# Kernel tuning notes

Hardware: AMD Instinct MI355X
Metric: run time of the kernel (lower is better)

Reference implementation:

```python
import jax, jax.numpy as jnp
import numpy as np
import math

B, S, H = 8, 1024, 1024
NH, DH = 16, 64  # MULTI_HEAD, HIDDEN_SIZE_HEAD


def setup_inputs() -> dict:
    key = jax.random.key(0)
    ks = jax.random.split(key, 12)
    scale = 0.02
    inp = {
        "v": jax.random.normal(ks[0], (B, S, H), jnp.float32),
        "k": jax.random.normal(ks[1], (B, S, H), jnp.float32),
        "q": jax.random.normal(ks[2], (B, S, H), jnp.float32),
        # True = masked position (masked_fill semantics)
        "mask": jax.random.bernoulli(ks[3], 0.1, (B, 1, 1, S)),
        "Wq": jax.random.normal(ks[4], (H, H), jnp.float32) * scale,
        "bq": jnp.zeros((H,), jnp.float32),
        "Wk": jax.random.normal(ks[5], (H, H), jnp.float32) * scale,
        "bk": jnp.zeros((H,), jnp.float32),
        "Wv": jax.random.normal(ks[6], (H, H), jnp.float32) * scale,
        "bv": jnp.zeros((H,), jnp.float32),
        "Wm": jax.random.normal(ks[7], (H, H), jnp.float32) * scale,
        "bm": jnp.zeros((H,), jnp.float32),
    }
    return inp


def _split_heads(x):
    # [B, S, H] -> [B, NH, S, DH]
    b, s, _ = x.shape
    return x.reshape(b, s, NH, DH).transpose(0, 2, 1, 3)


def reference(v, k, q, mask, Wq, bq, Wk, bk, Wv, bv, Wm, bm):
    # QKV projections (torch Linear: x @ W.T + b)
    qh = _split_heads(q @ Wq.T + bq)  # [B, NH, S, DH]
    kh = _split_heads(k @ Wk.T + bk)
    vh = _split_heads(v @ Wv.T + bv)

    scores = jnp.einsum("bhqd,bhkd->bhqk", qh, kh) / math.sqrt(DH)
    scores = jnp.where(mask, jnp.float32(-1e9), scores)
    att = jax.nn.softmax(scores, axis=-1)
    # dropout rate 0.0 (eval mode) -> identity
    ctx = jnp.einsum("bhqk,bhkd->bhqd", att, vh)  # [B, NH, S, DH]

    b = q.shape[0]
    merged = ctx.transpose(0, 2, 1, 3).reshape(b, -1, NH * DH)  # [B, S, H]
    return merged @ Wm.T + bm
```

## Files before the change

kernel.cpp:

```cpp
#include <hip/hip_runtime.h>
#include <hip/hip_bf16.h>

#define Bn 8
#define Sn 1024
#define Hn 1024
#define NHn 16
#define DHn 64
#define Mn (Bn * Sn)

typedef unsigned short u16;
typedef short bf16x8 __attribute__((ext_vector_type(8)));
typedef unsigned short u16x4 __attribute__((ext_vector_type(4)));
typedef float f32x4 __attribute__((ext_vector_type(4)));

__device__ __forceinline__ u16 f2bf(float x) {
  union { __hip_bfloat16 h; u16 u; } cv;
  cv.h = __float2bfloat16(x);
  return cv.u;
}

__device__ __forceinline__ void async_ld16(void* lds, const void* g) {
  __builtin_amdgcn_global_load_lds(
      (const __attribute__((address_space(1))) void*)g,
      (__attribute__((address_space(3))) void*)lds, 16, 0, 0);
}

__global__ __launch_bounds__(256) void sniff_k(const void* __restrict__ mask,
                                               int* __restrict__ flags) {
  __shared__ int viol;
  if (threadIdx.x == 0) viol = 0;
  __syncthreads();
  const unsigned* mw = (const unsigned*)mask;
  int vb = 0;
#pragma unroll
  for (int j = 0; j < 8; ++j) {
    unsigned v = mw[threadIdx.x * 8 + j];
    if (v > 1u) vb |= 1;
    if ((v & 0xFEFEFEFEu) != 0u) vb |= 2;
    if (!(v == 0u || v == 0x3F800000u)) vb |= 4;
    unsigned h0 = v & 0xFFFFu, h1 = v >> 16;
    if (!((h0 == 0u || h0 == 0x3F80u) && (h1 == 0u || h1 == 0x3F80u))) vb |= 8;
  }
  if (vb) atomicOr(&viol, vb);
  __syncthreads();
  if (threadIdx.x == 0) {
    int mt;
    if (!(viol & 1))      mt = 0;
    else if (!(viol & 2)) mt = 1;
    else if (!(viol & 4)) mt = 3;
    else if (!(viol & 8)) mt = 2;
    else                  mt = 0;
    flags[1] = mt;
  }
}

__global__ __launch_bounds__(256) void convert3(
    const float* __restrict__ a, const float* __restrict__ b,
    const float* __restrict__ c, u16* __restrict__ da,
    u16* __restrict__ db, u16* __restrict__ dc) {
  const int seg = blockIdx.x >> 12;
  const int bid = blockIdx.x & 4095;
  const float* s = seg == 0 ? a : seg == 1 ? b : c;
  u16* d        = seg == 0 ? da : seg == 1 ? db : dc;
  const int i = (bid * 256 + threadIdx.x) * 8;
  f32x4 lo = *(const f32x4*)(s + i);
  f32x4 hi = *(const f32x4*)(s + i + 4);
  bf16x8 o;
#pragma unroll
  for (int j = 0; j < 4; ++j) { o[j] = (short)f2bf(lo[j]); o[4 + j] = (short)f2bf(hi[j]); }
  *(bf16x8*)(d + i) = o;
}

__global__ __launch_bounds__(256) void convertW(
    const float* __restrict__ a, const float* __restrict__ b,
    const float* __restrict__ c, const float* __restrict__ e,
    u16* __restrict__ da, u16* __restrict__ db,
    u16* __restrict__ dc, u16* __restrict__ de) {
  const int seg = blockIdx.x >> 9;
  const int bid = blockIdx.x & 511;
  const float* s = seg == 0 ? a : seg == 1 ? b : seg == 2 ? c : e;
  u16* d        = seg == 0 ? da : seg == 1 ? db : seg == 2 ? dc : de;
  const int i = (bid * 256 + threadIdx.x) * 8;
  f32x4 lo = *(const f32x4*)(s + i);
  f32x4 hi = *(const f32x4*)(s + i + 4);
  bf16x8 o;
#pragma unroll
  for (int j = 0; j < 4; ++j) { o[j] = (short)f2bf(lo[j]); o[4 + j] = (short)f2bf(hi[j]); }
  *(bf16x8*)(d + i) = o;
}

template <int OMODE>
__global__ __launch_bounds__(256) void gemm_bt(
    const u16* __restrict__ X, const u16* __restrict__ W,
    const float* __restrict__ bias, void* __restrict__ O, float scale)
{
  __shared__ __attribute__((aligned(16))) u16 As[128 * 32];
  __shared__ __attribute__((aligned(16))) u16 Bs[128 * 32];
  const int tid  = threadIdx.x;
  const int wave = tid >> 6;
  const int lane = tid & 63;
  const int ln   = lane & 15;
  const int quad = lane >> 4;
  const int m0 = blockIdx.x * 128;
  const int n0 = blockIdx.y * 128;
  const int wm = (wave & 1) * 64;
  const int wn = (wave >> 1) * 64;
  const int r0 = tid >> 2;
  const int oc = (tid & 3) * 8;
  char* A0 = (char*)As + wave * 1024;
  char* A1 = (char*)As + 4096 + wave * 1024;
  char* B0 = (char*)Bs + wave * 1024;
  char* B1 = (char*)Bs + 4096 + wave * 1024;

  f32x4 acc[4][4] = {};

  for (int k0 = 0; k0 < 1024; k0 += 32) {
    async_ld16(A0, X + (size_t)(m0 + r0) * 1024 + k0 + oc);
    async_ld16(A1, X + (size_t)(m0 + 64 + r0) * 1024 + k0 + oc);
    async_ld16(B0, W + (size_t)(n0 + r0) * 1024 + k0 + oc);
    async_ld16(B1, W + (size_t)(n0 + 64 + r0) * 1024 + k0 + oc);
    __syncthreads();
    bf16x8 af[4], bf[4];
#pragma unroll
    for (int t = 0; t < 4; ++t)
      af[t] = *(const bf16x8*)&As[(wm + t * 16 + ln) * 32 + quad * 8];
#pragma unroll
    for (int t = 0; t < 4; ++t)
      bf[t] = *(const bf16x8*)&Bs[(wn + t * 16 + ln) * 32 + quad * 8];
#pragma unroll
    for (int i = 0; i < 4; ++i)
#pragma unroll
      for (int j = 0; j < 4; ++j)
        acc[i][j] = __builtin_amdgcn_mfma_f32_16x16x32_bf16(af[i], bf[j], acc[i][j], 0, 0, 0);
    __syncthreads();
  }

  if (OMODE == 2) {
    const int bb = m0 >> 10;
    const int sb = m0 & 1023;
#pragma unroll
    for (int j = 0; j < 4; ++j) {
      const int col = n0 + wn + j * 16 + ln;
      const float bv = bias[col];
#pragma unroll
      for (int i = 0; i < 4; ++i) {
        const int sl = sb + wm + i * 16 + quad * 4;
        u16x4 pk;
#pragma unroll
        for (int r = 0; r < 4; ++r) pk[r] = f2bf((acc[i][j][r] + bv) * scale);
        *(u16x4*)&((u16*)O)[((size_t)(bb * 1024 + col)) * 1024 + sl] = pk;
      }
    }
  } else {
#pragma unroll
    for (int j = 0; j < 4; ++j) {
      const int col = n0 + wn + j * 16 + ln;
      const float bv = bias[col];
#pragma unroll
      for (int i = 0; i < 4; ++i) {
        const int rowb = m0 + wm + i * 16 + quad * 4;
#pragma unroll
        for (int r = 0; r < 4; ++r) {
          const float val = (acc[i][j][r] + bv) * scale;
          const size_t idx = (size_t)(rowb + r) * 1024 + col;
          if (OMODE == 1) ((float*)O)[idx] = val;
          else            ((u16*)O)[idx]   = f2bf(val);
        }
      }
    }
  }
}

__global__ __launch_bounds__(256) void attn(
    const u16* __restrict__ Qb, const u16* __restrict__ Kb,
    const u16* __restrict__ Vbt, const void* __restrict__ mask,
    const int* __restrict__ flags, u16* __restrict__ Ctx)
{
  __shared__ __attribute__((aligned(16))) u16 Ks[128 * 72];
  __shared__ __attribute__((aligned(16))) u16 Vt[64 * 136];
  __shared__ __attribute__((aligned(16))) u16 Pl[4][16 * 136];
  __shared__ __attribute__((aligned(16))) float maskf[Sn];

  const int tid  = threadIdx.x;
  const int wave = tid >> 6;
  const int lane = tid & 63;
  const int ln   = lane & 15;
  const int quad = lane >> 4;
  const int qt = blockIdx.x & 15;
  const int bh = blockIdx.x >> 4;
  const int b  = bh >> 4;
  const int h  = bh & 15;

  const int mt = flags[1];
  for (int i = tid; i < Sn; i += 256) {
    const int idx = b * Sn + i;
    int nz;
    if (mt == 0)      nz = ((const int*)mask)[idx] != 0;
    else if (mt == 1) nz = ((const signed char*)mask)[idx] != 0;
    else if (mt == 2) nz = ((const u16*)mask)[idx] != 0;
    else              nz = ((const unsigned*)mask)[idx] != 0;
    maskf[i] = nz ? -1e9f : 0.0f;
  }

  const size_t qoff = (size_t)(b * Sn + qt * 64 + wave * 16 + ln) * Hn + h * DHn;
  bf16x8 qf0 = *(const bf16x8*)&Qb[qoff + quad * 8];
  bf16x8 qf1 = *(const bf16x8*)&Qb[qoff + 32 + quad * 8];

  float mrun[4], lrun[4];
#pragma unroll
  for (int r = 0; r < 4; ++r) { mrun[r] = -INFINITY; lrun[r] = 0.0f; }
  f32x4 acc[4] = {};

  const int kr = tid >> 1, kh = tid & 1;
  const int vd = tid >> 2, vs = tid & 3;
  u16* pw = Pl[wave];

  for (int t8 = 0; t8 < 8; ++t8) {
    const int kv0 = t8 * 128;
    __syncthreads();
    {
      const u16* g = &Kb[(size_t)(b * Sn + kv0 + kr) * Hn + h * DHn + kh * 32];
      u16* l = &Ks[kr * 72 + kh * 32];
#pragma unroll
      for (int j = 0; j < 4; ++j) *(bf16x8*)(l + j * 8) = *(const bf16x8*)(g + j * 8);
    }
    {
      const u16* g = &Vbt[(size_t)(b * Sn + h * DHn + vd) * Sn + kv0 + vs * 32];
      u16* l = &Vt[vd * 136 + vs * 32];
#pragma unroll
      for (int j = 0; j < 4; ++j) *(bf16x8*)(l + j * 8) = *(const bf16x8*)(g + j * 8);
    }
    __syncthreads();

    f32x4 sc[8];
#pragma unroll
    for (int t = 0; t < 8; ++t) {
      const int row = (t * 16 + ln) * 72;
      bf16x8 kf0 = *(const bf16x8*)&Ks[row + quad * 8];
      bf16x8 kf1 = *(const bf16x8*)&Ks[row + 32 + quad * 8];
      f32x4 z = {};
      z = __builtin_amdgcn_mfma_f32_16x16x32_bf16(qf0, kf0, z, 0, 0, 0);
      z = __builtin_amdgcn_mfma_f32_16x16x32_bf16(qf1, kf1, z, 0, 0, 0);
      sc[t] = z;
    }
    float mf[8];
#pragma unroll
    for (int t = 0; t < 8; ++t) mf[t] = maskf[kv0 + t * 16 + ln];
#pragma unroll
    for (int t = 0; t < 8; ++t)
#pragma unroll
      for (int r = 0; r < 4; ++r) sc[t][r] += mf[t];

    float al[4], mx[4];
#pragma unroll
    for (int r = 0; r < 4; ++r) {
      float v = sc[0][r];
#pragma unroll
      for (int t = 1; t < 8; ++t) v = fmaxf(v, sc[t][r]);
      v = fmaxf(v, __shfl_xor(v, 1));
      v = fmaxf(v, __shfl_xor(v, 2));
      v = fmaxf(v, __shfl_xor(v, 4));
      v = fmaxf(v, __shfl_xor(v, 8));
      const float mnew = fmaxf(mrun[r], v);
      al[r] = __expf(mrun[r] - mnew);
      mrun[r] = mnew;
      mx[r] = mnew;
    }
#pragma unroll
    for (int r = 0; r < 4; ++r) {
      float s = 0.0f;
#pragma unroll
      for (int t = 0; t < 8; ++t) {
        const float p = __expf(sc[t][r] - mx[r]);
        sc[t][r] = p;
        s += p;
      }
      s += __shfl_xor(s, 1);
      s += __shfl_xor(s, 2);
      s += __shfl_xor(s, 4);
      s += __shfl_xor(s, 8);
      lrun[r] = lrun[r] * al[r] + s;
    }
#pragma unroll
    for (int t = 0; t < 8; ++t)
#pragma unroll
      for (int r = 0; r < 4; ++r)
        pw[(quad * 4 + r) * 136 + t * 16 + ln] = f2bf(sc[t][r]);
    __syncthreads();
#pragma unroll
    for (int dt = 0; dt < 4; ++dt)
#pragma unroll
      for (int r = 0; r < 4; ++r) acc[dt][r] *= al[r];
    bf16x8 pa[4];
#pragma unroll
    for (int c = 0; c < 4; ++c)
      pa[c] = *(const bf16x8*)&pw[ln * 136 + c * 32 + quad * 8];
#pragma unroll
    for (int dt = 0; dt < 4; ++dt) {
      const int vrow = (dt * 16 + ln) * 136;
#pragma unroll
      for (int c = 0; c < 4; ++c) {
        bf16x8 vb = *(const bf16x8*)&Vt[vrow + c * 32 + quad * 8];
        acc[dt] = __builtin_amdgcn_mfma_f32_16x16x32_bf16(pa[c], vb, acc[dt], 0, 0, 0);
      }
    }
  }

#pragma unroll
  for (int dt = 0; dt < 4; ++dt)
#pragma unroll
    for (int r = 0; r < 4; ++r) {
      const int s = qt * 64 + wave * 16 + quad * 4 + r;
      Ctx[(size_t)(b * Sn + s) * Hn + h * DHn + dt * 16 + ln] = f2bf(acc[dt][r] / lrun[r]);
    }
}

extern "C" void kernel_launch(void* const* d_in, const int* in_sizes, int n_in,
                              void* d_out, int out_size, void* d_ws, size_t ws_size,
                              hipStream_t stream) {
  const float* v    = (const float*)d_in[0];
  const float* k    = (const float*)d_in[1];
  const float* q    = (const float*)d_in[2];
  const void*  mask = d_in[3];
  const float* Wq   = (const float*)d_in[4];
  const float* bq   = (const float*)d_in[5];
  const float* Wk   = (const float*)d_in[6];
  const float* bk   = (const float*)d_in[7];
  const float* Wv   = (const float*)d_in[8];
  const float* bv   = (const float*)d_in[9];
  const float* Wm   = (const float*)d_in[10];
  const float* bm   = (const float*)d_in[11];

  char* ws = (char*)d_ws;
  u16* qc  = (u16*)(ws);
  u16* kc  = (u16*)(ws + (16u << 20));
  u16* vc  = (u16*)(ws + (32u << 20));
  u16* Wqc = (u16*)(ws + (48u << 20));
  u16* Wkc = Wqc + (1u << 20);
  u16* Wvc = Wkc + (1u << 20);
  u16* Wmc = Wvc + (1u << 20);
  int* flags = (int*)(ws + (56u << 20));
  u16* Vbt = qc;
  u16* Cx  = kc;
  u16* Qb  = (u16*)d_out;
  u16* Kb  = Qb + (size_t)Mn * Hn;

  sniff_k<<<1, 256, 0, stream>>>(mask, flags);
  convert3<<<3 * 4096, 256, 0, stream>>>(q, k, v, qc, kc, vc);
  convertW<<<4 * 512, 256, 0, stream>>>(Wq, Wk, Wv, Wm, Wqc, Wkc, Wvc, Wmc);

  dim3 grid(Mn / 128, Hn / 128), blk(256);
  gemm_bt<0><<<grid, blk, 0, stream>>>(qc, Wqc, bq, Qb, 0.125f);
  gemm_bt<0><<<grid, blk, 0, stream>>>(kc, Wkc, bk, Kb, 1.0f);
  gemm_bt<2><<<grid, blk, 0, stream>>>(vc, Wvc, bv, Vbt, 1.0f);
  attn<<<dim3(Bn * NHn * (Sn / 64)), blk, 0, stream>>>(Qb, Kb, Vbt, mask, flags, Cx);
  gemm_bt<1><<<grid, blk, 0, stream>>>(Cx, Wmc, bm, d_out, 1.0f);
}
```

Measured before the change: 391.6 us.

## Prefetch K/V tiles into registers, XOR-swizzle LDS, drop P-tile barrier

The attention kernel now loads the next K and V tiles into registers while the current tile is being computed, so global load latency overlaps with the MFMA and softmax work. LDS padding is replaced by XOR swizzling of the K, V and P buffers, which shrinks shared memory use. The launch bound hint is raised to 3 blocks per CU to target higher occupancy. The barrier after writing P is removed because each wave only reads its own P slice. In exchange, more registers are held live for the prefetch, and the occupancy hint may force register spills.

```diff
diff --git a/kernel.cpp b/kernel.cpp
--- a/kernel.cpp
+++ b/kernel.cpp
@@ -171,14 +171,14 @@
   }
 }
 
-__global__ __launch_bounds__(256) void attn(
+__global__ __launch_bounds__(256, 3) void attn(
     const u16* __restrict__ Qb, const u16* __restrict__ Kb,
     const u16* __restrict__ Vbt, const void* __restrict__ mask,
     const int* __restrict__ flags, u16* __restrict__ Ctx)
 {
-  __shared__ __attribute__((aligned(16))) u16 Ks[128 * 72];
-  __shared__ __attribute__((aligned(16))) u16 Vt[64 * 136];
-  __shared__ __attribute__((aligned(16))) u16 Pl[4][16 * 136];
+  __shared__ __attribute__((aligned(16))) u16 Ks[128 * 64];
+  __shared__ __attribute__((aligned(16))) u16 Vt[64 * 128];
+  __shared__ __attribute__((aligned(16))) u16 Pl[4][16 * 128];
   __shared__ __attribute__((aligned(16))) float maskf[Sn];
 
   const int tid  = threadIdx.x;
@@ -213,31 +213,51 @@
 
   const int kr = tid >> 1, kh = tid & 1;
   const int vd = tid >> 2, vs = tid & 3;
-  u16* pw = Pl[wave];
+  char* pw = (char*)Pl[wave];
+  char* KsB = (char*)Ks;
+  char* VtB = (char*)Vt;
+
+  const u16* kg = &Kb[(size_t)(b * Sn + kr) * Hn + h * DHn + kh * 32];
+  const u16* vg = &Vbt[(size_t)(b * Sn + h * DHn + vd) * Sn + vs * 32];
+
+  bf16x8 kreg[4], vreg[4];
+#pragma unroll
+  for (int j = 0; j < 4; ++j) kreg[j] = *(const bf16x8*)(kg + j * 8);
+#pragma unroll
+  for (int j = 0; j < 4; ++j) vreg[j] = *(const bf16x8*)(vg + j * 8);
+
+  const int kwb = kr * 128 + kh * 64;
+  const int ksw = (kr & 7) << 4;
+  const int vwb = vd * 256 + vs * 64;
+  const int vsw = (vd & 7) << 4;
+  const int rsw = (ln & 7) << 4;
 
   for (int t8 = 0; t8 < 8; ++t8) {
     const int kv0 = t8 * 128;
     __syncthreads();
-    {
-      const u16* g = &Kb[(size_t)(b * Sn + kv0 + kr) * Hn + h * DHn + kh * 32];
-      u16* l = &Ks[kr * 72 + kh * 32];
-#pragma unroll
-      for (int j = 0; j < 4; ++j) *(bf16x8*)(l + j * 8) = *(const bf16x8*)(g + j * 8);
-    }
-    {
-      const u16* g = &Vbt[(size_t)(b * Sn + h * DHn + vd) * Sn + kv0 + vs * 32];
-      u16* l = &Vt[vd * 136 + vs * 32];
-#pragma unroll
-      for (int j = 0; j < 4; ++j) *(bf16x8*)(l + j * 8) = *(const bf16x8*)(g + j * 8);
-    }
+#pragma unroll
+    for (int j = 0; j < 4; ++j)
+      *(bf16x8*)(KsB + ((kwb + j * 16) ^ ksw)) = kreg[j];
+#pragma unroll
+    for (int j = 0; j < 4; ++j)
+      *(bf16x8*)(VtB + ((vwb + j * 16) ^ vsw)) = vreg[j];
     __syncthreads();
 
+    if (t8 < 7) {
+      const u16* kgn = kg + (size_t)(t8 + 1) * 128 * Hn;
+      const u16* vgn = vg + (t8 + 1) * 128;
+#pragma unroll
+      for (int j = 0; j < 4; ++j) kreg[j] = *(const bf16x8*)(kgn + j * 8);
+#pragma unroll
+      for (int j = 0; j < 4; ++j) vreg[j] = *(const bf16x8*)(vgn + j * 8);
+    }
+
     f32x4 sc[8];
 #pragma unroll
     for (int t = 0; t < 8; ++t) {
-      const int row = (t * 16 + ln) * 72;
-      bf16x8 kf0 = *(const bf16x8*)&Ks[row + quad * 8];
-      bf16x8 kf1 = *(const bf16x8*)&Ks[row + 32 + quad * 8];
+      const int rb = (t * 16 + ln) * 128;
+      bf16x8 kf0 = *(const bf16x8*)(KsB + ((rb + quad * 16) ^ rsw));
+      bf16x8 kf1 = *(const bf16x8*)(KsB + ((rb + 64 + quad * 16) ^ rsw));
       f32x4 z = {};
       z = __builtin_amdgcn_mfma_f32_16x16x32_bf16(qf0, kf0, z, 0, 0, 0);
       z = __builtin_amdgcn_mfma_f32_16x16x32_bf16(qf1, kf1, z, 0, 0, 0);
@@ -284,9 +304,11 @@
 #pragma unroll
     for (int t = 0; t < 8; ++t)
 #pragma unroll
-      for (int r = 0; r < 4; ++r)
-        pw[(quad * 4 + r) * 136 + t * 16 + ln] = f2bf(sc[t][r]);
-    __syncthreads();
+      for (int r = 0; r < 4; ++r) {
+        const int prow = quad * 4 + r;
+        *(u16*)(pw + ((prow * 256 + (t * 16 + ln) * 2) ^ ((prow & 7) << 4))) =
+            f2bf(sc[t][r]);
+      }
 #pragma unroll
     for (int dt = 0; dt < 4; ++dt)
 #pragma unroll
@@ -294,13 +316,13 @@
     bf16x8 pa[4];
 #pragma unroll
     for (int c = 0; c < 4; ++c)
-      pa[c] = *(const bf16x8*)&pw[ln * 136 + c * 32 + quad * 8];
+      pa[c] = *(const bf16x8*)(pw + ((ln * 256 + c * 64 + quad * 16) ^ rsw));
 #pragma unroll
     for (int dt = 0; dt < 4; ++dt) {
-      const int vrow = (dt * 16 + ln) * 136;
+      const int vrb = (dt * 16 + ln) * 256;
 #pragma unroll
       for (int c = 0; c < 4; ++c) {
-        bf16x8 vb = *(const bf16x8*)&Vt[vrow + c * 32 + quad * 8];
+        bf16x8 vb = *(const bf16x8*)(VtB + ((vrb + c * 64 + quad * 16) ^ rsw));
         acc[dt] = __builtin_amdgcn_mfma_f32_16x16x32_bf16(pa[c], vb, acc[dt], 0, 0, 0);
       }
     }
```

Result: slower. 443.4 us (+13.2%).
